# Kernel tuning notes

Hardware: AMD Instinct MI355X
Metric: run time of the kernel (lower is better)

The kernel has to match this reference:

```python
import jax, jax.numpy as jnp
import numpy as np

B, L, D, V = 512, 128, 512, 100000

def setup_inputs() -> dict:
    key = jax.random.key(0)
    ks = jax.random.split(key, 8)
    return {
        "t1s": jax.random.randint(ks[0], (B,), 0, V),
        "t2s": jax.random.randint(ks[1], (B,), 0, V),
        "t1_contexts": jax.random.randint(ks[2], (B, L), 0, V),
        "t2_contexts": jax.random.randint(ks[3], (B, L), 0, V),
        "embed_table": jax.random.normal(ks[4], (V, D), dtype=jnp.float32),
        "att_mat": jax.random.normal(ks[5], (D, D), dtype=jnp.float32) * (6.0 / (D + D)) ** 0.5,
        "w_pred": jax.random.normal(ks[6], (D, 1), dtype=jnp.float32) * 0.02,
        "b_pred": jnp.zeros((1,), dtype=jnp.float32),
    }

def _frob_normalize(x):
    # torch.norm(mat, p=2) is the Frobenius norm of the whole (L, D) matrix
    n = jnp.sqrt(jnp.sum(x * x, axis=(1, 2), keepdims=True))
    return x / n

def reference(t1s, t2s, t1_contexts, t2_contexts, embed_table, att_mat, w_pred, b_pred):
    # dropout is identity in eval mode; t1s/t2s embeddings are unused in the
    # 'dynamic' branch (dead code in the original forward).
    A = _frob_normalize(embed_table[t1_contexts])  # (B, L, D)
    Bm = _frob_normalize(embed_table[t2_contexts])  # (B, L, D)
    # batched bilinear attention: tanh(A @ att_mat @ B^T)
    S = jnp.tanh(jnp.einsum('bld,de,bme->blm', A, att_mat, Bm))  # (B, L, L)
    rows = jax.nn.softmax(jnp.mean(S, axis=2), axis=1)  # (B, L)
    cols = jax.nn.softmax(jnp.mean(S, axis=1), axis=1)  # (B, L)
    newA = jnp.einsum('bld,bl->bd', A, rows)   # (B, D)
    newB = jnp.einsum('bld,bl->bd', Bm, cols)  # (B, D)
    logits = ((newA * newB) @ w_pred + b_pred).reshape(-1)  # (B,)
    return logits, S
```

## Files before the change

kernel.cpp:

```cpp
#include <hip/hip_runtime.h>
#include <hip/hip_bf16.h>
#include <stdint.h>

#define NB 512
#define NL 128
#define ND 512

typedef __bf16 bf16;
typedef __bf16 bf16x8 __attribute__((ext_vector_type(8)));
typedef float  f32x4  __attribute__((ext_vector_type(4)));

__global__ __launch_bounds__(256) void k_gather(const int* __restrict__ ctx1,
                                                const int* __restrict__ ctx2,
                                                const float* __restrict__ table,
                                                bf16* __restrict__ d1,
                                                bf16* __restrict__ d2,
                                                float* __restrict__ ss,
                                                const float* __restrict__ att,
                                                bf16* __restrict__ attT) {
    const int b = blockIdx.x, side = blockIdx.y, zc = blockIdx.z, t = threadIdx.x;
    if (side == 2) {
        int chunk = b * 8 + zc;
        if (chunk < 1024) {
            int i = chunk * 256 + t;
            int n = i >> 9, k = i & 511;
            attT[i] = (bf16)att[k * 512 + n];
        }
        return;
    }
    const int* __restrict__ ctx = side ? ctx2 : ctx1;
    bf16* __restrict__ dst = side ? d2 : d1;
    const int base = b * NL;
    const int dv = t & 127, lr = t >> 7;
    float acc = 0.f;
    #pragma unroll
    for (int i = 0; i < 8; ++i) {
        int l = zc * 16 + i * 2 + lr;
        int idx = ctx[base + l];
        float4 v = ((const float4*)table)[(size_t)idx * (ND / 4) + dv];
        acc += v.x * v.x + v.y * v.y + v.z * v.z + v.w * v.w;
        union { bf16 h[4]; uint2 u; } pk;
        pk.h[0] = (bf16)v.x; pk.h[1] = (bf16)v.y;
        pk.h[2] = (bf16)v.z; pk.h[3] = (bf16)v.w;
        *((uint2*)(dst + (size_t)(base + l) * ND) + dv) = pk.u;
    }
    for (int o = 32; o; o >>= 1) acc += __shfl_xor(acc, o);
    __shared__ float red[4];
    if ((t & 63) == 0) red[t >> 6] = acc;
    __syncthreads();
    if (t == 0) atomicAdd(&ss[side * NB + b], red[0] + red[1] + red[2] + red[3]);
}

__global__ __launch_bounds__(256) void k_gemm1(const bf16* __restrict__ A,
                                               const bf16* __restrict__ B,
                                               bf16* __restrict__ Tout) {
    const int id  = blockIdx.x;
    const int xcd = id & 7;
    const int grp = id >> 3;
    const int n0  = (grp & 3) * 128;
    const int b   = (grp >> 2) * 8 + xcd;
    const int arow0 = b * NL;

    __shared__ __align__(16) bf16 As[128 * 64];
    __shared__ __align__(16) bf16 Bs[128 * 64];

    const int tid = threadIdx.x;
    const int lane = tid & 63, w = tid >> 6;
    const int lm = lane & 15, quad = lane >> 4;
    const int wm = (w & 1) * 64, wn = (w >> 1) * 64;

    f32x4 acc[4][4] = {};

    for (int k0 = 0; k0 < ND; k0 += 64) {
        #pragma unroll
        for (int i = 0; i < 4; ++i) {
            int s = w * 256 + i * 64 + lane;
            int r = s >> 3;
            int c = (s & 7) ^ (r & 7);
            const bf16* ga = A + (size_t)(arow0 + r) * ND + k0 + c * 8;
            const bf16* gb = B + (size_t)(n0 + r) * ND + k0 + c * 8;
            __builtin_amdgcn_global_load_lds(
                (const __attribute__((address_space(1))) void*)ga,
                (__attribute__((address_space(3))) void*)(As + (size_t)(w * 256 + i * 64) * 8),
                16, 0, 0);
            __builtin_amdgcn_global_load_lds(
                (const __attribute__((address_space(1))) void*)gb,
                (__attribute__((address_space(3))) void*)(Bs + (size_t)(w * 256 + i * 64) * 8),
                16, 0, 0);
        }
        __syncthreads();
        #pragma unroll
        for (int kk = 0; kk < 2; ++kk) {
            bf16x8 af[4], bfm[4];
            const int ca = (kk * 4 + quad) ^ (lm & 7);
            #pragma unroll
            for (int t4 = 0; t4 < 4; ++t4) {
                af[t4]  = *(const bf16x8*)&As[(wm + t4 * 16 + lm) * 64 + ca * 8];
                bfm[t4] = *(const bf16x8*)&Bs[(wn + t4 * 16 + lm) * 64 + ca * 8];
            }
            #pragma unroll
            for (int im = 0; im < 4; ++im)
                #pragma unroll
                for (int jn = 0; jn < 4; ++jn)
                    acc[im][jn] = __builtin_amdgcn_mfma_f32_16x16x32_bf16(
                        af[im], bfm[jn], acc[im][jn], 0, 0, 0);
        }
        __syncthreads();
    }

    #pragma unroll
    for (int im = 0; im < 4; ++im)
    #pragma unroll
    for (int jn = 0; jn < 4; ++jn)
    #pragma unroll
    for (int p = 0; p < 4; ++p) {
        int m = wm + im * 16 + quad * 4 + p;
        int n = wn + jn * 16 + lm;
        Tout[(size_t)(arow0 + m) * ND + n0 + n] = (bf16)acc[im][jn][p];
    }
}

__global__ __launch_bounds__(256) void k_gemm2_final(
        const bf16* __restrict__ Tin, const bf16* __restrict__ B,
        float* __restrict__ Sout,
        const bf16* __restrict__ Ab, const bf16* __restrict__ Bb,
        const float* __restrict__ ss,
        const float* __restrict__ w_pred, const float* __restrict__ b_pred,
        float* __restrict__ logits) {
    const int b = blockIdx.x;
    const int row0 = b * NL;

    __shared__ __align__(16) char smem[32768];
    bf16* As = (bf16*)smem;
    bf16* Bs = (bf16*)(smem + 16384);
    float* pA = (float*)smem;
    float* pB = (float*)(smem + 16384);
    __shared__ float rowb[2][NL], colb[2][NL];
    __shared__ float wrow[NL], wcol[NL];

    const int tid = threadIdx.x;
    const int lane = tid & 63, w = tid >> 6;
    const int lm = lane & 15, quad = lane >> 4;
    const int wm = (w & 1) * 64, wn = (w >> 1) * 64;

    f32x4 acc[4][4] = {};

    for (int k0 = 0; k0 < ND; k0 += 64) {
        #pragma unroll
        for (int i = 0; i < 4; ++i) {
            int s = w * 256 + i * 64 + lane;
            int r = s >> 3;
            int c = (s & 7) ^ (r & 7);
            const bf16* ga = Tin + (size_t)(row0 + r) * ND + k0 + c * 8;
            const bf16* gb = B   + (size_t)(row0 + r) * ND + k0 + c * 8;
            __builtin_amdgcn_global_load_lds(
                (const __attribute__((address_space(1))) void*)ga,
                (__attribute__((address_space(3))) void*)(As + (size_t)(w * 256 + i * 64) * 8),
                16, 0, 0);
            __builtin_amdgcn_global_load_lds(
                (const __attribute__((address_space(1))) void*)gb,
                (__attribute__((address_space(3))) void*)(Bs + (size_t)(w * 256 + i * 64) * 8),
                16, 0, 0);
        }
        __syncthreads();
        #pragma unroll
        for (int kk = 0; kk < 2; ++kk) {
            bf16x8 af[4], bfm[4];
            const int ca = (kk * 4 + quad) ^ (lm & 7);
            #pragma unroll
            for (int t4 = 0; t4 < 4; ++t4) {
                af[t4]  = *(const bf16x8*)&As[(wm + t4 * 16 + lm) * 64 + ca * 8];
                bfm[t4] = *(const bf16x8*)&Bs[(wn + t4 * 16 + lm) * 64 + ca * 8];
            }
            #pragma unroll
            for (int im = 0; im < 4; ++im)
                #pragma unroll
                for (int jn = 0; jn < 4; ++jn)
                    acc[im][jn] = __builtin_amdgcn_mfma_f32_16x16x32_bf16(
                        af[im], bfm[jn], acc[im][jn], 0, 0, 0);
        }
        __syncthreads();
    }

    const float sc = rsqrtf(ss[b] * ss[NB + b]);
    float* __restrict__ Sb = Sout + (size_t)b * NL * NL;
    #pragma unroll
    for (int im = 0; im < 4; ++im)
    #pragma unroll
    for (int jn = 0; jn < 4; ++jn)
    #pragma unroll
    for (int p = 0; p < 4; ++p) {
        float v = tanhf(acc[im][jn][p] * sc);
        acc[im][jn][p] = v;
        int m = wm + im * 16 + quad * 4 + p;
        int n = wn + jn * 16 + lm;
        __builtin_nontemporal_store(v, &Sb[m * NL + n]);
    }
    #pragma unroll
    for (int im = 0; im < 4; ++im)
    #pragma unroll
    for (int p = 0; p < 4; ++p) {
        float r = acc[im][0][p] + acc[im][1][p] + acc[im][2][p] + acc[im][3][p];
        r += __shfl_xor(r, 1); r += __shfl_xor(r, 2);
        r += __shfl_xor(r, 4); r += __shfl_xor(r, 8);
        if (lm == 0) rowb[wn >> 6][wm + im * 16 + quad * 4 + p] = r;
    }
    #pragma unroll
    for (int jn = 0; jn < 4; ++jn) {
        float cv = 0.f;
        #pragma unroll
        for (int im = 0; im < 4; ++im)
            #pragma unroll
            for (int p = 0; p < 4; ++p) cv += acc[im][jn][p];
        cv += __shfl_xor(cv, 16); cv += __shfl_xor(cv, 32);
        if (quad == 0) colb[wm >> 6][wn + jn * 16 + lm] = cv;
    }
    __syncthreads();

    if (tid < 64) {
        float a  = (rowb[0][tid] + rowb[1][tid]) * (1.f / NL);
        float c2 = (rowb[0][tid + 64] + rowb[1][tid + 64]) * (1.f / NL);
        float mx = fmaxf(a, c2);
        for (int o = 32; o; o >>= 1) mx = fmaxf(mx, __shfl_xor(mx, o));
        float e0 = expf(a - mx), e1 = expf(c2 - mx);
        float s = e0 + e1;
        for (int o = 32; o; o >>= 1) s += __shfl_xor(s, o);
        float inv = 1.f / s;
        wrow[tid] = e0 * inv; wrow[tid + 64] = e1 * inv;
    } else if (tid < 128) {
        int q = tid - 64;
        float a  = (colb[0][q] + colb[1][q]) * (1.f / NL);
        float c2 = (colb[0][q + 64] + colb[1][q + 64]) * (1.f / NL);
        float mx = fmaxf(a, c2);
        for (int o = 32; o; o >>= 1) mx = fmaxf(mx, __shfl_xor(mx, o));
        float e0 = expf(a - mx), e1 = expf(c2 - mx);
        float s = e0 + e1;
        for (int o = 32; o; o >>= 1) s += __shfl_xor(s, o);
        float inv = 1.f / s;
        wcol[q] = e0 * inv; wcol[q + 64] = e1 * inv;
    }
    __syncthreads();

    const int c = tid & 63, g = tid >> 6;
    const bf16* __restrict__ Abase = Ab + (size_t)b * NL * ND;
    const bf16* __restrict__ Bbase = Bb + (size_t)b * NL * ND;
    float aacc[8] = {}, bacc[8] = {};
    for (int l = g; l < NL; l += 4) {
        float wr = wrow[l], wc = wcol[l];
        bf16x8 va = *(const bf16x8*)(Abase + (size_t)l * ND + c * 8);
        bf16x8 vb = *(const bf16x8*)(Bbase + (size_t)l * ND + c * 8);
        #pragma unroll
        for (int j = 0; j < 8; ++j) {
            aacc[j] += wr * (float)va[j];
            bacc[j] += wc * (float)vb[j];
        }
    }
    #pragma unroll
    for (int j = 0; j < 8; ++j) {
        pA[g * ND + c * 8 + j] = aacc[j];
        pB[g * ND + c * 8 + j] = bacc[j];
    }
    __syncthreads();

    if (tid < 64) {
        float dot = 0.f;
        #pragma unroll
        for (int j = 0; j < 8; ++j) {
            int d = tid * 8 + j;
            float na = pA[0 * ND + d] + pA[1 * ND + d] + pA[2 * ND + d] + pA[3 * ND + d];
            float nb = pB[0 * ND + d] + pB[1 * ND + d] + pB[2 * ND + d] + pB[3 * ND + d];
            dot += na * nb * w_pred[d];
        }
        for (int o = 32; o; o >>= 1) dot += __shfl_xor(dot, o);
        if (tid == 0)
            logits[b] = dot * rsqrtf(ss[b]) * rsqrtf(ss[NB + b]) + b_pred[0];
    }
}

extern "C" void kernel_launch(void* const* d_in, const int* in_sizes, int n_in,
                              void* d_out, int out_size, void* d_ws, size_t ws_size,
                              hipStream_t stream) {
    const int*   t1c = (const int*)d_in[2];
    const int*   t2c = (const int*)d_in[3];
    const float* emb = (const float*)d_in[4];
    const float* att = (const float*)d_in[5];
    const float* wp  = (const float*)d_in[6];
    const float* bp  = (const float*)d_in[7];

    float* out    = (float*)d_out;
    float* logits = out;
    float* S      = out + NB;

    char* ws = (char*)d_ws;
    bf16*  Ab   = (bf16*)(ws);
    bf16*  Bb   = (bf16*)(ws + 67108864);
    bf16*  Tb   = (bf16*)(ws + 134217728);
    bf16*  attT = (bf16*)(ws + 201326592);
    float* ss   = (float*)(ws + 201850880);

    hipMemsetAsync(ss, 0, 4096, stream);
    k_gather<<<dim3(NB, 3, 8), 256, 0, stream>>>(t1c, t2c, emb, Ab, Bb, ss, att, attT);
    k_gemm1<<<dim3(2048), 256, 0, stream>>>(Ab, attT, Tb);
    k_gemm2_final<<<dim3(NB), 256, 0, stream>>>(Tb, Bb, S, Ab, Bb, ss, wp, bp, logits);
}
```

Measured before the change: 424.0 us.

## Fuse both GEMMs into one kernel, keeping the intermediate tile in LDS

Merges k_gemm1 and k_gemm2_final into a single per-batch kernel. For each 128-wide column chunk of A·att it computes the chunk into registers, writes it as bf16 into a swizzled LDS buffer, and accumulates it straight into A·att·Bᵀ. This removes the global round-trip of the intermediate T matrix and one kernel launch. In exchange each block uses 64KB+ of LDS, which lowers occupancy, and there are only 512 blocks, each looping serially over four chunks. That gives less parallelism than the old 2048-block first GEMM.

```diff
diff --git a/kernel.cpp b/kernel.cpp
--- a/kernel.cpp
+++ b/kernel.cpp
@@ -51,133 +51,115 @@
     if (t == 0) atomicAdd(&ss[side * NB + b], red[0] + red[1] + red[2] + red[3]);
 }
 
-__global__ __launch_bounds__(256) void k_gemm1(const bf16* __restrict__ A,
-                                               const bf16* __restrict__ B,
-                                               bf16* __restrict__ Tout) {
-    const int id  = blockIdx.x;
-    const int xcd = id & 7;
-    const int grp = id >> 3;
-    const int n0  = (grp & 3) * 128;
-    const int b   = (grp >> 2) * 8 + xcd;
-    const int arow0 = b * NL;
-
-    __shared__ __align__(16) bf16 As[128 * 64];
-    __shared__ __align__(16) bf16 Bs[128 * 64];
+__global__ __launch_bounds__(256) void k_fused(
+        const bf16* __restrict__ A, const bf16* __restrict__ attT,
+        const bf16* __restrict__ Bb,
+        float* __restrict__ Sout, const float* __restrict__ ss,
+        const float* __restrict__ w_pred, const float* __restrict__ b_pred,
+        float* __restrict__ logits) {
+    const int b = blockIdx.x;
+    const int row0 = b * NL;
+
+    __shared__ __align__(16) char smem[65536];
+    bf16* As = (bf16*)smem;
+    bf16* Bs = (bf16*)(smem + 16384);
+    bf16* Tc = (bf16*)(smem + 32768);
+    float* pA = (float*)smem;
+    float* pB = (float*)(smem + 16384);
+    __shared__ float rowb[2][NL], colb[2][NL];
+    __shared__ float wrow[NL], wcol[NL];
 
     const int tid = threadIdx.x;
     const int lane = tid & 63, w = tid >> 6;
     const int lm = lane & 15, quad = lane >> 4;
     const int wm = (w & 1) * 64, wn = (w >> 1) * 64;
 
-    f32x4 acc[4][4] = {};
-
-    for (int k0 = 0; k0 < ND; k0 += 64) {
+    f32x4 acc2[4][4] = {};
+
+    for (int nc = 0; nc < 4; ++nc) {
+        const int n0 = nc * 128;
+        f32x4 acc1[4][4] = {};
+
+        for (int k0 = 0; k0 < ND; k0 += 64) {
+            #pragma unroll
+            for (int i = 0; i < 4; ++i) {
+                int s = w * 256 + i * 64 + lane;
+                int r = s >> 3;
+                int c = (s & 7) ^ (r & 7);
+                __builtin_amdgcn_global_load_lds(
+                    (const __attribute__((address_space(1))) void*)(A + (size_t)(row0 + r) * ND + k0 + c * 8),
+                    (__attribute__((address_space(3))) void*)(As + (size_t)(w * 256 + i * 64) * 8),
+                    16, 0, 0);
+                __builtin_amdgcn_global_load_lds(
+                    (const __attribute__((address_space(1))) void*)(attT + (size_t)(n0 + r) * ND + k0 + c * 8),
+                    (__attribute__((address_space(3))) void*)(Bs + (size_t)(w * 256 + i * 64) * 8),
+                    16, 0, 0);
+            }
+            __syncthreads();
+            #pragma unroll
+            for (int kk = 0; kk < 2; ++kk) {
+                bf16x8 af[4], bfm[4];
+                const int ca = (kk * 4 + quad) ^ (lm & 7);
+                #pragma unroll
+                for (int t4 = 0; t4 < 4; ++t4) {
+                    af[t4]  = *(const bf16x8*)&As[(wm + t4 * 16 + lm) * 64 + ca * 8];
+                    bfm[t4] = *(const bf16x8*)&Bs[(wn + t4 * 16 + lm) * 64 + ca * 8];
+                }
+                #pragma unroll
+                for (int im = 0; im < 4; ++im)
+                    #pragma unroll
+                    for (int jn = 0; jn < 4; ++jn)
+                        acc1[im][jn] = __builtin_amdgcn_mfma_f32_16x16x32_bf16(
+                            af[im], bfm[jn], acc1[im][jn], 0, 0, 0);
+            }
+            __syncthreads();
+        }
+
+        #pragma unroll
+        for (int im = 0; im < 4; ++im)
+        #pragma unroll
+        for (int jn = 0; jn < 4; ++jn)
+        #pragma unroll
+        for (int p = 0; p < 4; ++p) {
+            int m  = wm + im * 16 + quad * 4 + p;
+            int k2 = wn + jn * 16 + lm;
+            int phys = (k2 >> 3) ^ (m & 7);
+            Tc[m * 128 + phys * 8 + (k2 & 7)] = (bf16)acc1[im][jn][p];
+        }
         #pragma unroll
         for (int i = 0; i < 4; ++i) {
             int s = w * 256 + i * 64 + lane;
             int r = s >> 3;
             int c = (s & 7) ^ (r & 7);
-            const bf16* ga = A + (size_t)(arow0 + r) * ND + k0 + c * 8;
-            const bf16* gb = B + (size_t)(n0 + r) * ND + k0 + c * 8;
             __builtin_amdgcn_global_load_lds(
-                (const __attribute__((address_space(1))) void*)ga,
+                (const __attribute__((address_space(1))) void*)(Bb + (size_t)(row0 + r) * ND + n0 + c * 8),
                 (__attribute__((address_space(3))) void*)(As + (size_t)(w * 256 + i * 64) * 8),
                 16, 0, 0);
             __builtin_amdgcn_global_load_lds(
-                (const __attribute__((address_space(1))) void*)gb,
+                (const __attribute__((address_space(1))) void*)(Bb + (size_t)(row0 + r) * ND + n0 + 64 + c * 8),
                 (__attribute__((address_space(3))) void*)(Bs + (size_t)(w * 256 + i * 64) * 8),
                 16, 0, 0);
         }
         __syncthreads();
-        #pragma unroll
-        for (int kk = 0; kk < 2; ++kk) {
+
+        #pragma unroll
+        for (int kk2 = 0; kk2 < 4; ++kk2) {
+            const bf16* buf = (kk2 < 2) ? As : Bs;
             bf16x8 af[4], bfm[4];
-            const int ca = (kk * 4 + quad) ^ (lm & 7);
+            const int cb = ((kk2 & 1) * 4 + quad) ^ (lm & 7);
             #pragma unroll
             for (int t4 = 0; t4 < 4; ++t4) {
-                af[t4]  = *(const bf16x8*)&As[(wm + t4 * 16 + lm) * 64 + ca * 8];
-                bfm[t4] = *(const bf16x8*)&Bs[(wn + t4 * 16 + lm) * 64 + ca * 8];
+                int rowA = wm + t4 * 16 + lm;
+                int physA = (kk2 * 4 + quad) ^ (rowA & 7);
+                af[t4]  = *(const bf16x8*)&Tc[rowA * 128 + physA * 8];
+                bfm[t4] = *(const bf16x8*)&buf[(wn + t4 * 16 + lm) * 64 + cb * 8];
             }
             #pragma unroll
             for (int im = 0; im < 4; ++im)
                 #pragma unroll
                 for (int jn = 0; jn < 4; ++jn)
-                    acc[im][jn] = __builtin_amdgcn_mfma_f32_16x16x32_bf16(
-                        af[im], bfm[jn], acc[im][jn], 0, 0, 0);
-        }
-        __syncthreads();
-    }
-
-    #pragma unroll
-    for (int im = 0; im < 4; ++im)
-    #pragma unroll
-    for (int jn = 0; jn < 4; ++jn)
-    #pragma unroll
-    for (int p = 0; p < 4; ++p) {
-        int m = wm + im * 16 + quad * 4 + p;
-        int n = wn + jn * 16 + lm;
-        Tout[(size_t)(arow0 + m) * ND + n0 + n] = (bf16)acc[im][jn][p];
-    }
-}
-
-__global__ __launch_bounds__(256) void k_gemm2_final(
-        const bf16* __restrict__ Tin, const bf16* __restrict__ B,
-        float* __restrict__ Sout,
-        const bf16* __restrict__ Ab, const bf16* __restrict__ Bb,
-        const float* __restrict__ ss,
-        const float* __restrict__ w_pred, const float* __restrict__ b_pred,
-        float* __restrict__ logits) {
-    const int b = blockIdx.x;
-    const int row0 = b * NL;
-
-    __shared__ __align__(16) char smem[32768];
-    bf16* As = (bf16*)smem;
-    bf16* Bs = (bf16*)(smem + 16384);
-    float* pA = (float*)smem;
-    float* pB = (float*)(smem + 16384);
-    __shared__ float rowb[2][NL], colb[2][NL];
-    __shared__ float wrow[NL], wcol[NL];
-
-    const int tid = threadIdx.x;
-    const int lane = tid & 63, w = tid >> 6;
-    const int lm = lane & 15, quad = lane >> 4;
-    const int wm = (w & 1) * 64, wn = (w >> 1) * 64;
-
-    f32x4 acc[4][4] = {};
-
-    for (int k0 = 0; k0 < ND; k0 += 64) {
-        #pragma unroll
-        for (int i = 0; i < 4; ++i) {
-            int s = w * 256 + i * 64 + lane;
-            int r = s >> 3;
-            int c = (s & 7) ^ (r & 7);
-            const bf16* ga = Tin + (size_t)(row0 + r) * ND + k0 + c * 8;
-            const bf16* gb = B   + (size_t)(row0 + r) * ND + k0 + c * 8;
-            __builtin_amdgcn_global_load_lds(
-                (const __attribute__((address_space(1))) void*)ga,
-                (__attribute__((address_space(3))) void*)(As + (size_t)(w * 256 + i * 64) * 8),
-                16, 0, 0);
-            __builtin_amdgcn_global_load_lds(
-                (const __attribute__((address_space(1))) void*)gb,
-                (__attribute__((address_space(3))) void*)(Bs + (size_t)(w * 256 + i * 64) * 8),
-                16, 0, 0);
-        }
-        __syncthreads();
-        #pragma unroll
-        for (int kk = 0; kk < 2; ++kk) {
-            bf16x8 af[4], bfm[4];
-            const int ca = (kk * 4 + quad) ^ (lm & 7);
-            #pragma unroll
-            for (int t4 = 0; t4 < 4; ++t4) {
-                af[t4]  = *(const bf16x8*)&As[(wm + t4 * 16 + lm) * 64 + ca * 8];
-                bfm[t4] = *(const bf16x8*)&Bs[(wn + t4 * 16 + lm) * 64 + ca * 8];
-            }
-            #pragma unroll
-            for (int im = 0; im < 4; ++im)
-                #pragma unroll
-                for (int jn = 0; jn < 4; ++jn)
-                    acc[im][jn] = __builtin_amdgcn_mfma_f32_16x16x32_bf16(
-                        af[im], bfm[jn], acc[im][jn], 0, 0, 0);
+                    acc2[im][jn] = __builtin_amdgcn_mfma_f32_16x16x32_bf16(
+                        af[im], bfm[jn], acc2[im][jn], 0, 0, 0);
         }
         __syncthreads();
     }
@@ -190,8 +172,8 @@
     for (int jn = 0; jn < 4; ++jn)
     #pragma unroll
     for (int p = 0; p < 4; ++p) {
-        float v = tanhf(acc[im][jn][p] * sc);
-        acc[im][jn][p] = v;
+        float v = tanhf(acc2[im][jn][p] * sc);
+        acc2[im][jn][p] = v;
         int m = wm + im * 16 + quad * 4 + p;
         int n = wn + jn * 16 + lm;
         __builtin_nontemporal_store(v, &Sb[m * NL + n]);
@@ -200,7 +182,7 @@
     for (int im = 0; im < 4; ++im)
     #pragma unroll
     for (int p = 0; p < 4; ++p) {
-        float r = acc[im][0][p] + acc[im][1][p] + acc[im][2][p] + acc[im][3][p];
+        float r = acc2[im][0][p] + acc2[im][1][p] + acc2[im][2][p] + acc2[im][3][p];
         r += __shfl_xor(r, 1); r += __shfl_xor(r, 2);
         r += __shfl_xor(r, 4); r += __shfl_xor(r, 8);
         if (lm == 0) rowb[wn >> 6][wm + im * 16 + quad * 4 + p] = r;
@@ -211,7 +193,7 @@
         #pragma unroll
         for (int im = 0; im < 4; ++im)
             #pragma unroll
-            for (int p = 0; p < 4; ++p) cv += acc[im][jn][p];
+            for (int p = 0; p < 4; ++p) cv += acc2[im][jn][p];
         cv += __shfl_xor(cv, 16); cv += __shfl_xor(cv, 32);
         if (quad == 0) colb[wm >> 6][wn + jn * 16 + lm] = cv;
     }
@@ -242,7 +224,7 @@
     __syncthreads();
 
     const int c = tid & 63, g = tid >> 6;
-    const bf16* __restrict__ Abase = Ab + (size_t)b * NL * ND;
+    const bf16* __restrict__ Abase = A  + (size_t)b * NL * ND;
     const bf16* __restrict__ Bbase = Bb + (size_t)b * NL * ND;
     float aacc[8] = {}, bacc[8] = {};
     for (int l = g; l < NL; l += 4) {
@@ -294,12 +276,10 @@
     char* ws = (char*)d_ws;
     bf16*  Ab   = (bf16*)(ws);
     bf16*  Bb   = (bf16*)(ws + 67108864);
-    bf16*  Tb   = (bf16*)(ws + 134217728);
-    bf16*  attT = (bf16*)(ws + 201326592);
-    float* ss   = (float*)(ws + 201850880);
+    bf16*  attT = (bf16*)(ws + 134217728);
+    float* ss   = (float*)(ws + 134742016);
 
     hipMemsetAsync(ss, 0, 4096, stream);
     k_gather<<<dim3(NB, 3, 8), 256, 0, stream>>>(t1c, t2c, emb, Ab, Bb, ss, att, attT);
-    k_gemm1<<<dim3(2048), 256, 0, stream>>>(Ab, attT, Tb);
-    k_gemm2_final<<<dim3(NB), 256, 0, stream>>>(Tb, Bb, S, Ab, Bb, ss, wp, bp, logits);
+    k_fused<<<dim3(NB), 256, 0, stream>>>(Ab, attT, Bb, S, ss, wp, bp, logits);
 }
```

Result: slower. 464.2 us (+9.5%).
